# Kernel optimization log

Measured on AMD Instinct MI355X. Metric: run time of the kernel, lower is better.

The kernel has to match this reference:

```python
import jax, jax.numpy as jnp
import numpy as np

N_NODES = 4096
N_GRAPHS = 128
D_IN = 128
HEADS = 4
KEY_SIZE = 32  # == num_channels
D_OUT = 32 * D_IN  # num_channels * irreps.dim


def setup_inputs() -> dict:
    key = jax.random.key(0)
    ks = jax.random.split(key, 5)
    nodes = jax.random.normal(ks[0], (N_NODES, D_IN), dtype=jnp.float32)
    # 128 graphs of 32 nodes each, packed: sum(n_node) == N_NODES
    n_node = jnp.full((N_GRAPHS,), N_NODES // N_GRAPHS, dtype=jnp.int32)
    s_in = 1.0 / np.sqrt(D_IN)
    s_h = 1.0 / np.sqrt(HEADS * KEY_SIZE)
    Wq = jax.random.normal(ks[1], (D_IN, HEADS, KEY_SIZE), dtype=jnp.float32) * s_in
    Wk = jax.random.normal(ks[2], (D_IN, HEADS, KEY_SIZE), dtype=jnp.float32) * s_in
    Wv = jax.random.normal(ks[3], (D_IN, HEADS, KEY_SIZE), dtype=jnp.float32) * s_in
    Wo = jax.random.normal(ks[4], (HEADS * KEY_SIZE, D_OUT), dtype=jnp.float32) * s_h
    bq = jnp.zeros((HEADS, KEY_SIZE), dtype=jnp.float32)
    bk = jnp.zeros((HEADS, KEY_SIZE), dtype=jnp.float32)
    bv = jnp.zeros((HEADS, KEY_SIZE), dtype=jnp.float32)
    bo = jnp.zeros((D_OUT,), dtype=jnp.float32)
    return {"nodes": nodes, "n_node": n_node, "Wq": Wq, "bq": bq,
            "Wk": Wk, "bk": bk, "Wv": Wv, "bv": bv, "Wo": Wo, "bo": bo}


def reference(nodes, n_node, Wq, bq, Wk, bk, Wv, bv, Wo, bo):
    N = nodes.shape[0]
    G = n_node.shape[0]
    # segment id per packed node (get_segment_ids)
    seg = jnp.repeat(jnp.arange(G), n_node, total_repeat_length=N)
    # per-head projections: [N, H, K]
    q = jnp.einsum('nd,dhk->nhk', nodes, Wq) + bq
    k = jnp.einsum('nd,dhk->nhk', nodes, Wk) + bk
    v = jnp.einsum('nd,dhk->nhk', nodes, Wv) + bv
    # dense logits masked to block-diagonal per-graph blocks: [H, N, N]
    logits = jnp.einsum('nhk,mhk->hnm', q, k) / jnp.sqrt(jnp.float32(KEY_SIZE))
    mask = seg[:, None] == seg[None, :]  # [N, N]
    logits = jnp.where(mask[None, :, :], logits, jnp.float32(-1e30))
    attn = jax.nn.softmax(logits, axis=-1)
    out = jnp.einsum('hnm,mhk->nhk', attn, v).reshape(N, HEADS * KEY_SIZE)
    return out @ Wo + bo  # [N, num_channels * d_in]
```

## Files before the change

### kernel.cpp

```cpp
#include <hip/hip_runtime.h>
#include <hip/hip_bf16.h>


typedef __attribute__((ext_vector_type(4))) float f32x4;
typedef __attribute__((ext_vector_type(8))) short s16x8;
typedef __attribute__((ext_vector_type(4))) short s16x4;
typedef __attribute__((ext_vector_type(8))) __bf16 bf16x8;

static __device__ __forceinline__ short f2bf(float f) {
  union { float f; unsigned u; } v; v.f = f;
  unsigned r = v.u + 0x7fffu + ((v.u >> 16) & 1u);
  return (short)(r >> 16);
}

static __device__ __forceinline__ f32x4 mfma16(s16x8 a, s16x8 b, f32x4 c) {
  return __builtin_amdgcn_mfma_f32_16x16x32_bf16(
      __builtin_bit_cast(bf16x8, a), __builtin_bit_cast(bf16x8, b), c, 0, 0, 0);
}

__global__ __launch_bounds__(256) void k0_prep(
    const float* __restrict__ Wq, const float* __restrict__ Wk,
    const float* __restrict__ Wv, const float* __restrict__ Wo,
    unsigned short* __restrict__ WqkvT, unsigned short* __restrict__ WoT)
{
  __shared__ alignas(16) short sT[64][136];
  const int b = blockIdx.x;
  const float* in; unsigned short* out; int C; int n0;
  if (b < 64)      { in = Wo; out = WoT;           C = 4096; n0 = b << 6; }
  else if (b < 66) { in = Wq; out = WqkvT;         C = 128;  n0 = (b - 64) << 6; }
  else if (b < 68) { in = Wk; out = WqkvT + 16384; C = 128;  n0 = (b - 66) << 6; }
  else             { in = Wv; out = WqkvT + 32768; C = 128;  n0 = (b - 68) << 6; }
  const int t  = threadIdx.x;
  const int rr = t >> 4;
  const int c4 = (t & 15) << 2;
  #pragma unroll
  for (int i = 0; i < 8; ++i) {
    int r = i * 16 + rr;
    float4 v = *(const float4*)(in + r * C + n0 + c4);
    sT[c4 + 0][r] = f2bf(v.x);
    sT[c4 + 1][r] = f2bf(v.y);
    sT[c4 + 2][r] = f2bf(v.z);
    sT[c4 + 3][r] = f2bf(v.w);
  }
  __syncthreads();
  const int c  = t >> 2;
  const int k0 = (t & 3) << 5;
  #pragma unroll
  for (int j = 0; j < 4; ++j)
    *(s16x8*)&out[(n0 + c) * 128 + k0 + j * 8] = *(const s16x8*)&sT[c][k0 + j * 8];
}

__global__ __launch_bounds__(64) void k1_qkv_attn(
    const float* __restrict__ nodes,
    const unsigned short* __restrict__ WqkvT,
    const float* __restrict__ bq, const float* __restrict__ bk,
    const float* __restrict__ bv,
    unsigned short* __restrict__ attout)
{
  const int g = blockIdx.x;
  const int h = blockIdx.y;
  const int lane = threadIdx.x;
  const int l15 = lane & 15;
  const int qd = lane >> 4;

  __shared__ alignas(16) short sN[32][136];
  __shared__ alignas(16) short sQ[32][40];
  __shared__ alignas(16) short sK[32][40];
  __shared__ alignas(16) short sVT[32][40];
  __shared__ alignas(16) short sP[32][40];

  const float* ng = nodes + g * 32 * 128;
  #pragma unroll
  for (int i = 0; i < 16; ++i) {
    int f4  = i * 64 + lane;
    int row = f4 >> 5;
    int c4  = (f4 & 31) << 2;
    float4 v = *(const float4*)(ng + row * 128 + c4);
    s16x4 p;
    p[0] = f2bf(v.x); p[1] = f2bf(v.y); p[2] = f2bf(v.z); p[3] = f2bf(v.w);
    *(s16x4*)&sN[row][c4] = p;
  }
  __syncthreads();

  s16x8 afrag[2][4];
  #pragma unroll
  for (int mt = 0; mt < 2; ++mt)
    #pragma unroll
    for (int kk = 0; kk < 4; ++kk)
      afrag[mt][kk] = *(const s16x8*)&sN[mt * 16 + l15][kk * 32 + qd * 8];

  const float* Bm[3] = {bq, bk, bv};

  #pragma unroll
  for (int m3 = 0; m3 < 3; ++m3) {
    const unsigned short* WT = WqkvT + m3 * 16384;
    s16x8 bfr[4][2];
    #pragma unroll
    for (int kk = 0; kk < 4; ++kk)
      #pragma unroll
      for (int nt = 0; nt < 2; ++nt)
        bfr[kk][nt] = *(const s16x8*)&WT[(h * 32 + nt * 16 + l15) * 128 + kk * 32 + qd * 8];
    f32x4 acc[2][2];
    f32x4 zero = {0.f, 0.f, 0.f, 0.f};
    acc[0][0] = zero; acc[0][1] = zero; acc[1][0] = zero; acc[1][1] = zero;
    #pragma unroll
    for (int kk = 0; kk < 4; ++kk)
      #pragma unroll
      for (int mt = 0; mt < 2; ++mt)
        #pragma unroll
        for (int nt = 0; nt < 2; ++nt)
          acc[mt][nt] = mfma16(afrag[mt][kk], bfr[kk][nt], acc[mt][nt]);
    float b0 = Bm[m3][h * 32 + l15];
    float b1 = Bm[m3][h * 32 + 16 + l15];
    #pragma unroll
    for (int mt = 0; mt < 2; ++mt)
      #pragma unroll
      for (int nt = 0; nt < 2; ++nt) {
        float bb = nt ? b1 : b0;
        #pragma unroll
        for (int r = 0; r < 4; ++r) {
          int m = mt * 16 + qd * 4 + r;
          int c = nt * 16 + l15;
          float val = acc[mt][nt][r] + bb;
          if (m3 == 0)      sQ[m][c]  = f2bf(val * 0.17677669529663687f);
          else if (m3 == 1) sK[m][c]  = f2bf(val);
          else              sVT[c][m] = f2bf(val);
        }
      }
  }
  __syncthreads();

  s16x8 qf[2], kf[2];
  #pragma unroll
  for (int mt = 0; mt < 2; ++mt) qf[mt] = *(const s16x8*)&sQ[mt * 16 + l15][qd * 8];
  #pragma unroll
  for (int nt = 0; nt < 2; ++nt) kf[nt] = *(const s16x8*)&sK[nt * 16 + l15][qd * 8];
  f32x4 sacc[2][2];
  {
    f32x4 zero = {0.f, 0.f, 0.f, 0.f};
    #pragma unroll
    for (int mt = 0; mt < 2; ++mt)
      #pragma unroll
      for (int nt = 0; nt < 2; ++nt)
        sacc[mt][nt] = mfma16(qf[mt], kf[nt], zero);
  }

  #pragma unroll
  for (int mt = 0; mt < 2; ++mt)
    #pragma unroll
    for (int r = 0; r < 4; ++r) {
      float a0 = sacc[mt][0][r], a1 = sacc[mt][1][r];
      float mx = fmaxf(a0, a1);
      mx = fmaxf(mx, __shfl_xor(mx, 1, 64));
      mx = fmaxf(mx, __shfl_xor(mx, 2, 64));
      mx = fmaxf(mx, __shfl_xor(mx, 4, 64));
      mx = fmaxf(mx, __shfl_xor(mx, 8, 64));
      float e0 = __expf(a0 - mx), e1 = __expf(a1 - mx);
      float s = e0 + e1;
      s += __shfl_xor(s, 1, 64);
      s += __shfl_xor(s, 2, 64);
      s += __shfl_xor(s, 4, 64);
      s += __shfl_xor(s, 8, 64);
      float inv = 1.0f / s;
      int m = mt * 16 + qd * 4 + r;
      sP[m][l15]      = f2bf(e0 * inv);
      sP[m][16 + l15] = f2bf(e1 * inv);
    }
  __syncthreads();

  s16x8 pf[2], vf[2];
  #pragma unroll
  for (int mt = 0; mt < 2; ++mt) pf[mt] = *(const s16x8*)&sP[mt * 16 + l15][qd * 8];
  #pragma unroll
  for (int nt = 0; nt < 2; ++nt) vf[nt] = *(const s16x8*)&sVT[nt * 16 + l15][qd * 8];
  f32x4 oacc[2][2];
  {
    f32x4 zero = {0.f, 0.f, 0.f, 0.f};
    #pragma unroll
    for (int mt = 0; mt < 2; ++mt)
      #pragma unroll
      for (int nt = 0; nt < 2; ++nt)
        oacc[mt][nt] = mfma16(pf[mt], vf[nt], zero);
  }
  unsigned short* ao = attout + (g * 32) * 128 + h * 32;
  #pragma unroll
  for (int mt = 0; mt < 2; ++mt)
    #pragma unroll
    for (int nt = 0; nt < 2; ++nt)
      #pragma unroll
      for (int r = 0; r < 4; ++r) {
        int m = mt * 16 + qd * 4 + r;
        int c = nt * 16 + l15;
        ao[m * 128 + c] = (unsigned short)f2bf(oacc[mt][nt][r]);
      }
}

__global__ __launch_bounds__(256) void k3_gemm(
    const unsigned short* __restrict__ A,
    const unsigned short* __restrict__ BT,
    const float* __restrict__ bo,
    float* __restrict__ C)
{
  __shared__ alignas(16) short sA[128][136];
  __shared__ alignas(16) short sB[128][136];
  const int t  = threadIdx.x;
  const int m0 = blockIdx.y << 7;
  const int n0 = blockIdx.x << 7;

  #pragma unroll
  for (int i = 0; i < 8; ++i) {
    int id  = i * 256 + t;
    int row = id >> 4;
    int ch  = (id & 15) << 3;
    *(s16x8*)&sA[row][ch] = *(const s16x8*)(A  + (m0 + row) * 128 + ch);
    *(s16x8*)&sB[row][ch] = *(const s16x8*)(BT + (n0 + row) * 128 + ch);
  }
  __syncthreads();

  const int w    = t >> 6;
  const int lane = t & 63;
  const int l15  = lane & 15;
  const int qd   = lane >> 4;
  const int wm   = (w >> 1) << 6;
  const int wn   = (w & 1) << 6;

  f32x4 acc[4][4];
  {
    f32x4 zero = {0.f, 0.f, 0.f, 0.f};
    #pragma unroll
    for (int i = 0; i < 4; ++i)
      #pragma unroll
      for (int j = 0; j < 4; ++j) acc[i][j] = zero;
  }

  #pragma unroll
  for (int kk = 0; kk < 4; ++kk) {
    s16x8 af[4], bf[4];
    #pragma unroll
    for (int i = 0; i < 4; ++i)
      af[i] = *(const s16x8*)&sA[wm + i * 16 + l15][kk * 32 + qd * 8];
    #pragma unroll
    for (int j = 0; j < 4; ++j)
      bf[j] = *(const s16x8*)&sB[wn + j * 16 + l15][kk * 32 + qd * 8];
    #pragma unroll
    for (int i = 0; i < 4; ++i)
      #pragma unroll
      for (int j = 0; j < 4; ++j)
        acc[i][j] = mfma16(af[i], bf[j], acc[i][j]);
  }

  float bov[4];
  #pragma unroll
  for (int j = 0; j < 4; ++j) bov[j] = bo[n0 + wn + j * 16 + l15];

  #pragma unroll
  for (int i = 0; i < 4; ++i) {
    int rbase = m0 + wm + i * 16 + qd * 4;
    #pragma unroll
    for (int r = 0; r < 4; ++r) {
      float* crow = C + (rbase + r) * 4096 + n0 + wn + l15;
      #pragma unroll
      for (int j = 0; j < 4; ++j)
        crow[j * 16] = acc[i][j][r] + bov[j];
    }
  }
}

extern "C" void kernel_launch(void* const* d_in, const int* in_sizes, int n_in,
                              void* d_out, int out_size, void* d_ws, size_t ws_size,
                              hipStream_t stream) {
  const float* nodes = (const float*)d_in[0];
  const float* Wq = (const float*)d_in[2];
  const float* bq = (const float*)d_in[3];
  const float* Wk = (const float*)d_in[4];
  const float* bk = (const float*)d_in[5];
  const float* Wv = (const float*)d_in[6];
  const float* bv = (const float*)d_in[7];
  const float* Wo = (const float*)d_in[8];
  const float* bo = (const float*)d_in[9];
  float* out = (float*)d_out;

  unsigned short* attout = (unsigned short*)d_ws;
  unsigned short* WoT    = attout + 4096 * 128;
  unsigned short* WqkvT  = WoT + 4096 * 128;

  k0_prep<<<70, 256, 0, stream>>>(Wq, Wk, Wv, Wo, WqkvT, WoT);
  k1_qkv_attn<<<dim3(128, 4), 64, 0, stream>>>(nodes, WqkvT, bq, bk, bv, attout);
  k3_gemm<<<dim3(32, 32), 256, 0, stream>>>(attout, WoT, bo, out);
}
```

Measured before the change: 109.2 us.

## Vectorize output stores via transposed MFMA and pair heads per attention block

The output GEMM now computes the transposed product (B×A), so each lane holds four consecutive output columns. It writes them as 16-byte nontemporal stores with a vectorized bias load, replacing scalar strided stores. The attention kernel uses the same operand swap to pack its bf16 outputs into 8-byte stores. It also processes two heads per 128-thread block, which halves the redundant node-tile loads and conversions. The large fp32 output write dominates, so wider stores target memory efficiency, and nontemporal stores may change cache behaviour.

Result: slower. 112.3 us (+2.9%).

```diff
diff --git a/kernel.cpp b/kernel.cpp
--- a/kernel.cpp
+++ b/kernel.cpp
@@ -50,7 +50,7 @@
     *(s16x8*)&out[(n0 + c) * 128 + k0 + j * 8] = *(const s16x8*)&sT[c][k0 + j * 8];
 }
 
-__global__ __launch_bounds__(64) void k1_qkv_attn(
+__global__ __launch_bounds__(128) void k1_qkv_attn(
     const float* __restrict__ nodes,
     const unsigned short* __restrict__ WqkvT,
     const float* __restrict__ bq, const float* __restrict__ bk,
@@ -58,21 +58,22 @@
     unsigned short* __restrict__ attout)
 {
   const int g = blockIdx.x;
-  const int h = blockIdx.y;
-  const int lane = threadIdx.x;
+  const int w = threadIdx.x >> 6;
+  const int h = blockIdx.y * 2 + w;
+  const int lane = threadIdx.x & 63;
   const int l15 = lane & 15;
-  const int qd = lane >> 4;
+  const int qd  = lane >> 4;
 
   __shared__ alignas(16) short sN[32][136];
-  __shared__ alignas(16) short sQ[32][40];
-  __shared__ alignas(16) short sK[32][40];
-  __shared__ alignas(16) short sVT[32][40];
-  __shared__ alignas(16) short sP[32][40];
+  __shared__ alignas(16) short sQ[2][32][40];
+  __shared__ alignas(16) short sK[2][32][40];
+  __shared__ alignas(16) short sVT[2][32][40];
+  __shared__ alignas(16) short sP[2][32][40];
 
   const float* ng = nodes + g * 32 * 128;
   #pragma unroll
-  for (int i = 0; i < 16; ++i) {
-    int f4  = i * 64 + lane;
+  for (int i = 0; i < 8; ++i) {
+    int f4  = i * 128 + threadIdx.x;
     int row = f4 >> 5;
     int c4  = (f4 & 31) << 2;
     float4 v = *(const float4*)(ng + row * 128 + c4);
@@ -122,9 +123,9 @@
           int m = mt * 16 + qd * 4 + r;
           int c = nt * 16 + l15;
           float val = acc[mt][nt][r] + bb;
-          if (m3 == 0)      sQ[m][c]  = f2bf(val * 0.17677669529663687f);
-          else if (m3 == 1) sK[m][c]  = f2bf(val);
-          else              sVT[c][m] = f2bf(val);
+          if (m3 == 0)      sQ[w][m][c]  = f2bf(val * 0.17677669529663687f);
+          else if (m3 == 1) sK[w][m][c]  = f2bf(val);
+          else              sVT[w][c][m] = f2bf(val);
         }
       }
   }
@@ -132,9 +133,9 @@
 
   s16x8 qf[2], kf[2];
   #pragma unroll
-  for (int mt = 0; mt < 2; ++mt) qf[mt] = *(const s16x8*)&sQ[mt * 16 + l15][qd * 8];
-  #pragma unroll
-  for (int nt = 0; nt < 2; ++nt) kf[nt] = *(const s16x8*)&sK[nt * 16 + l15][qd * 8];
+  for (int mt = 0; mt < 2; ++mt) qf[mt] = *(const s16x8*)&sQ[w][mt * 16 + l15][qd * 8];
+  #pragma unroll
+  for (int nt = 0; nt < 2; ++nt) kf[nt] = *(const s16x8*)&sK[w][nt * 16 + l15][qd * 8];
   f32x4 sacc[2][2];
   {
     f32x4 zero = {0.f, 0.f, 0.f, 0.f};
@@ -163,36 +164,35 @@
       s += __shfl_xor(s, 8, 64);
       float inv = 1.0f / s;
       int m = mt * 16 + qd * 4 + r;
-      sP[m][l15]      = f2bf(e0 * inv);
-      sP[m][16 + l15] = f2bf(e1 * inv);
+      sP[w][m][l15]      = f2bf(e0 * inv);
+      sP[w][m][16 + l15] = f2bf(e1 * inv);
     }
   __syncthreads();
 
   s16x8 pf[2], vf[2];
   #pragma unroll
-  for (int mt = 0; mt < 2; ++mt) pf[mt] = *(const s16x8*)&sP[mt * 16 + l15][qd * 8];
-  #pragma unroll
-  for (int nt = 0; nt < 2; ++nt) vf[nt] = *(const s16x8*)&sVT[nt * 16 + l15][qd * 8];
-  f32x4 oacc[2][2];
+  for (int mt = 0; mt < 2; ++mt) pf[mt] = *(const s16x8*)&sP[w][mt * 16 + l15][qd * 8];
+  #pragma unroll
+  for (int nt = 0; nt < 2; ++nt) vf[nt] = *(const s16x8*)&sVT[w][nt * 16 + l15][qd * 8];
+  f32x4 oaccT[2][2];
   {
     f32x4 zero = {0.f, 0.f, 0.f, 0.f};
     #pragma unroll
-    for (int mt = 0; mt < 2; ++mt)
-      #pragma unroll
-      for (int nt = 0; nt < 2; ++nt)
-        oacc[mt][nt] = mfma16(pf[mt], vf[nt], zero);
+    for (int nt = 0; nt < 2; ++nt)
+      #pragma unroll
+      for (int mt = 0; mt < 2; ++mt)
+        oaccT[nt][mt] = mfma16(vf[nt], pf[mt], zero);
   }
   unsigned short* ao = attout + (g * 32) * 128 + h * 32;
   #pragma unroll
-  for (int mt = 0; mt < 2; ++mt)
-    #pragma unroll
-    for (int nt = 0; nt < 2; ++nt)
-      #pragma unroll
-      for (int r = 0; r < 4; ++r) {
-        int m = mt * 16 + qd * 4 + r;
-        int c = nt * 16 + l15;
-        ao[m * 128 + c] = (unsigned short)f2bf(oacc[mt][nt][r]);
-      }
+  for (int nt = 0; nt < 2; ++nt)
+    #pragma unroll
+    for (int mt = 0; mt < 2; ++mt) {
+      s16x4 pk;
+      #pragma unroll
+      for (int r = 0; r < 4; ++r) pk[r] = f2bf(oaccT[nt][mt][r]);
+      *(s16x4*)&ao[(mt * 16 + l15) * 128 + nt * 16 + qd * 4] = pk;
+    }
 }
 
 __global__ __launch_bounds__(256) void k3_gemm(
@@ -228,9 +228,9 @@
   {
     f32x4 zero = {0.f, 0.f, 0.f, 0.f};
     #pragma unroll
-    for (int i = 0; i < 4; ++i)
-      #pragma unroll
-      for (int j = 0; j < 4; ++j) acc[i][j] = zero;
+    for (int j = 0; j < 4; ++j)
+      #pragma unroll
+      for (int i = 0; i < 4; ++i) acc[j][i] = zero;
   }
 
   #pragma unroll
@@ -243,25 +243,20 @@
     for (int j = 0; j < 4; ++j)
       bf[j] = *(const s16x8*)&sB[wn + j * 16 + l15][kk * 32 + qd * 8];
     #pragma unroll
-    for (int i = 0; i < 4; ++i)
-      #pragma unroll
-      for (int j = 0; j < 4; ++j)
-        acc[i][j] = mfma16(af[i], bf[j], acc[i][j]);
-  }
-
-  float bov[4];
-  #pragma unroll
-  for (int j = 0; j < 4; ++j) bov[j] = bo[n0 + wn + j * 16 + l15];
-
-  #pragma unroll
-  for (int i = 0; i < 4; ++i) {
-    int rbase = m0 + wm + i * 16 + qd * 4;
-    #pragma unroll
-    for (int r = 0; r < 4; ++r) {
-      float* crow = C + (rbase + r) * 4096 + n0 + wn + l15;
-      #pragma unroll
-      for (int j = 0; j < 4; ++j)
-        crow[j * 16] = acc[i][j][r] + bov[j];
+    for (int j = 0; j < 4; ++j)
+      #pragma unroll
+      for (int i = 0; i < 4; ++i)
+        acc[j][i] = mfma16(bf[j], af[i], acc[j][i]);
+  }
+
+  #pragma unroll
+  for (int j = 0; j < 4; ++j) {
+    f32x4 bb = *(const f32x4*)&bo[n0 + wn + j * 16 + qd * 4];
+    #pragma unroll
+    for (int i = 0; i < 4; ++i) {
+      f32x4 v = acc[j][i] + bb;
+      float* p = C + (size_t)(m0 + wm + i * 16 + l15) * 4096 + n0 + wn + j * 16 + qd * 4;
+      __builtin_nontemporal_store(v, (f32x4*)p);
     }
   }
 }
@@ -285,6 +280,6 @@
   unsigned short* WqkvT  = WoT + 4096 * 128;
 
   k0_prep<<<70, 256, 0, stream>>>(Wq, Wk, Wv, Wo, WqkvT, WoT);
-  k1_qkv_attn<<<dim3(128, 4), 64, 0, stream>>>(nodes, WqkvT, bq, bk, bv, attout);
+  k1_qkv_attn<<<dim3(128, 2), 128, 0, stream>>>(nodes, WqkvT, bq, bk, bv, attout);
   k3_gemm<<<dim3(32, 32), 256, 0, stream>>>(attout, WoT, bo, out);
 }
```
